# Kernel optimization log

Hardware: AMD Instinct MI355X
Metric: run time of the kernel (lower is better)

## Reference

```python
import jax, jax.numpy as jnp
import numpy as np

B = 65536  # batch size


def setup_inputs() -> dict:
    key = jax.random.key(0)
    ks = jax.random.split(key, 8)
    x = jax.random.normal(ks[0], (B, 784), dtype=jnp.float32)
    conv_w = jax.random.normal(ks[1], (3, 3), dtype=jnp.float32)
    w1 = jax.random.normal(ks[2], (676, 256), dtype=jnp.float32) * 0.04
    b1 = jnp.zeros((256,), dtype=jnp.float32)
    w2 = jax.random.normal(ks[3], (256, 128), dtype=jnp.float32) * 0.06
    b2 = jnp.zeros((128,), dtype=jnp.float32)
    w3 = jax.random.normal(ks[4], (128, 10), dtype=jnp.float32) * 0.09
    b3 = jnp.zeros((10,), dtype=jnp.float32)
    return {"x": x, "conv_w": conv_w, "w1": w1, "b1": b1,
            "w2": w2, "b2": b2, "w3": w3, "b3": b3}


def reference(x, conv_w, w1, b1, w2, b2, w3, b3):
    # x: [B, 784] -> images [B, 1, 28, 28]
    img = x.reshape(-1, 1, 28, 28)
    # Convolve() is a valid cross-correlation (tensordot of window with kernel,
    # no flip) -> lax.conv_general_dilated (also no kernel flip).
    kern = conv_w.reshape(1, 1, 3, 3)  # [O, I, kh, kw]
    y = jax.lax.conv_general_dilated(
        img, kern, window_strides=(1, 1), padding="VALID",
        dimension_numbers=("NCHW", "OIHW", "NCHW"))  # [B, 1, 26, 26]
    h = y.reshape(y.shape[0], 26 * 26)
    h = jax.nn.relu(h @ w1 + b1)
    h = jax.nn.relu(h @ w2 + b2)
    return h @ w3 + b3  # [B, 10] logits
```

## Files before the change

kernel.cpp:

```cpp
#include <hip/hip_runtime.h>
#include <hip/hip_bf16.h>

typedef __bf16 bf16x8 __attribute__((ext_vector_type(8)));
typedef float  f32x4  __attribute__((ext_vector_type(4)));

#define B_ROWS 65536
#define MR 32
#define H0S 712
#define H1S 264
#define H2S 136
#define KC1 22
#define KC2 8
#define KC3 4

#define W1B_ELEMS (704*256)
#define W2B_ELEMS (256*128)
#define W3B_ELEMS (128*16)

__global__ void pack_weights(const float* __restrict__ w1,
                             const float* __restrict__ w2,
                             const float* __restrict__ w3,
                             __hip_bfloat16* __restrict__ w1b,
                             __hip_bfloat16* __restrict__ w2b,
                             __hip_bfloat16* __restrict__ w3b) {
    int idx = blockIdx.x * 256 + threadIdx.x;
    if (idx < W1B_ELEMS) {
        int ki = idx & 31, t = idx >> 5;
        int n = t & 255, kc = t >> 8;
        int k = kc * 32 + ki;
        float v = (k < 676) ? w1[k * 256 + n] : 0.0f;
        w1b[idx] = __float2bfloat16(v);
    } else if (idx < W1B_ELEMS + W2B_ELEMS) {
        int j = idx - W1B_ELEMS;
        int ki = j & 31, t = j >> 5;
        int n = t & 127, kc = t >> 7;
        w2b[j] = __float2bfloat16(w2[(kc * 32 + ki) * 128 + n]);
    } else if (idx < W1B_ELEMS + W2B_ELEMS + W3B_ELEMS) {
        int j = idx - W1B_ELEMS - W2B_ELEMS;
        int ki = j & 31, t = j >> 5;
        int n = t & 15, kc = t >> 4;
        float v = (n < 10) ? w3[(kc * 32 + ki) * 10 + n] : 0.0f;
        w3b[j] = __float2bfloat16(v);
    }
}

__global__ __launch_bounds__(256, 2)
void fused_model(const float* __restrict__ x, const float* __restrict__ cw,
                 const __hip_bfloat16* __restrict__ w1b, const float* __restrict__ b1,
                 const __hip_bfloat16* __restrict__ w2b, const float* __restrict__ b2,
                 const __hip_bfloat16* __restrict__ w3b, const float* __restrict__ b3,
                 float* __restrict__ out) {
    __shared__ __align__(16) char smem[MR * H0S * 2 + MR * H1S * 2];
    __hip_bfloat16* h0s = (__hip_bfloat16*)smem;
    __hip_bfloat16* h1s = (__hip_bfloat16*)(smem + MR * H0S * 2);
    __hip_bfloat16* h2s = (__hip_bfloat16*)smem;

    const int tid = threadIdx.x;
    const int r0  = blockIdx.x * MR;

    const float c00 = cw[0], c01 = cw[1], c02 = cw[2];
    const float c10 = cw[3], c11 = cw[4], c12 = cw[5];
    const float c20 = cw[6], c21 = cw[7], c22 = cw[8];

    for (int t = tid; t < MR * 26; t += 256) {
        int r = t / 26;
        int i = t - r * 26;
        const float* xr = x + (size_t)(r0 + r) * 784 + i * 28;
        float4 v[21];
        #pragma unroll
        for (int di = 0; di < 3; di++) {
            const float4* p4 = (const float4*)(xr + di * 28);
            #pragma unroll
            for (int q = 0; q < 7; q++) v[di * 7 + q] = p4[q];
        }
        #pragma unroll
        for (int k = 0; k < 21; k++)
            asm volatile("" :: "v"(v[k].x), "v"(v[k].y), "v"(v[k].z), "v"(v[k].w));
        float rb[3][28];
        #pragma unroll
        for (int di = 0; di < 3; di++) {
            #pragma unroll
            for (int q = 0; q < 7; q++) {
                rb[di][q*4+0] = v[di*7+q].x; rb[di][q*4+1] = v[di*7+q].y;
                rb[di][q*4+2] = v[di*7+q].z; rb[di][q*4+3] = v[di*7+q].w;
            }
        }
        __hip_bfloat162* hp = (__hip_bfloat162*)(h0s + r * H0S + i * 26);
        #pragma unroll
        for (int k = 0; k < 13; k++) {
            const int j0 = 2 * k, j1 = 2 * k + 1;
            float a0 = c00*rb[0][j0] + c01*rb[0][j0+1] + c02*rb[0][j0+2]
                     + c10*rb[1][j0] + c11*rb[1][j0+1] + c12*rb[1][j0+2]
                     + c20*rb[2][j0] + c21*rb[2][j0+1] + c22*rb[2][j0+2];
            float a1 = c00*rb[0][j1] + c01*rb[0][j1+1] + c02*rb[0][j1+2]
                     + c10*rb[1][j1] + c11*rb[1][j1+1] + c12*rb[1][j1+2]
                     + c20*rb[2][j1] + c21*rb[2][j1+1] + c22*rb[2][j1+2];
            __hip_bfloat162 pr;
            pr.x = __float2bfloat16(a0);
            pr.y = __float2bfloat16(a1);
            hp[k] = pr;
        }
    }
    for (int t = tid; t < MR * 18; t += 256) {
        int r = t / 18;
        int c = t - r * 18;
        ((uint*)(h0s + r * H0S + 676))[c] = 0u;
    }
    __syncthreads();

    const int wave = tid >> 6;
    const int lane = tid & 63;
    const int l15  = lane & 15;
    const int g    = lane >> 4;

    {
        f32x4 acc[2][4];
        #pragma unroll
        for (int mt = 0; mt < 2; mt++)
            #pragma unroll
            for (int nt = 0; nt < 4; nt++)
                acc[mt][nt] = (f32x4){0.f, 0.f, 0.f, 0.f};
        const int nb = wave * 64;
        bf16x8 ab[3][2], bb[3][4];
        #pragma unroll
        for (int p = 0; p < 2; p++) {
            #pragma unroll
            for (int mt = 0; mt < 2; mt++)
                ab[p][mt] = *(const bf16x8*)(h0s + (mt * 16 + l15) * H0S + p * 32 + g * 8);
            #pragma unroll
            for (int nt = 0; nt < 4; nt++)
                bb[p][nt] = *(const bf16x8*)(w1b + ((p * 256 + nb + nt * 16 + l15) * 32 + g * 8));
        }
        #pragma unroll
        for (int kc = 0; kc < KC1; kc++) {
            const int cur = kc % 3;
            const int nxt = (kc + 2) % 3;
            if (kc + 2 < KC1) {
                #pragma unroll
                for (int mt = 0; mt < 2; mt++)
                    ab[nxt][mt] = *(const bf16x8*)(h0s + (mt * 16 + l15) * H0S + (kc + 2) * 32 + g * 8);
                #pragma unroll
                for (int nt = 0; nt < 4; nt++)
                    bb[nxt][nt] = *(const bf16x8*)(w1b + (((kc + 2) * 256 + nb + nt * 16 + l15) * 32 + g * 8));
            }
            #pragma unroll
            for (int mt = 0; mt < 2; mt++)
                #pragma unroll
                for (int nt = 0; nt < 4; nt++)
                    acc[mt][nt] = __builtin_amdgcn_mfma_f32_16x16x32_bf16(
                        ab[cur][mt], bb[cur][nt], acc[mt][nt], 0, 0, 0);
        }
        #pragma unroll
        for (int nt = 0; nt < 4; nt++) {
            const int n = nb + nt * 16 + l15;
            const float bias = b1[n];
            #pragma unroll
            for (int mt = 0; mt < 2; mt++) {
                #pragma unroll
                for (int q = 0; q < 4; q++) {
                    const int row = mt * 16 + g * 4 + q;
                    float v = acc[mt][nt][q] + bias;
                    h1s[row * H1S + n] = __float2bfloat16(fmaxf(v, 0.0f));
                }
            }
        }
    }
    __syncthreads();

    {
        f32x4 acc[2][2];
        #pragma unroll
        for (int mt = 0; mt < 2; mt++)
            #pragma unroll
            for (int nt = 0; nt < 2; nt++)
                acc[mt][nt] = (f32x4){0.f, 0.f, 0.f, 0.f};
        const int nb = wave * 32;
        bf16x8 ab[3][2], bb[3][2];
        #pragma unroll
        for (int p = 0; p < 2; p++) {
            #pragma unroll
            for (int mt = 0; mt < 2; mt++)
                ab[p][mt] = *(const bf16x8*)(h1s + (mt * 16 + l15) * H1S + p * 32 + g * 8);
            #pragma unroll
            for (int nt = 0; nt < 2; nt++)
                bb[p][nt] = *(const bf16x8*)(w2b + ((p * 128 + nb + nt * 16 + l15) * 32 + g * 8));
        }
        #pragma unroll
        for (int kc = 0; kc < KC2; kc++) {
            const int cur = kc % 3;
            const int nxt = (kc + 2) % 3;
            if (kc + 2 < KC2) {
                #pragma unroll
                for (int mt = 0; mt < 2; mt++)
                    ab[nxt][mt] = *(const bf16x8*)(h1s + (mt * 16 + l15) * H1S + (kc + 2) * 32 + g * 8);
                #pragma unroll
                for (int nt = 0; nt < 2; nt++)
                    bb[nxt][nt] = *(const bf16x8*)(w2b + (((kc + 2) * 128 + nb + nt * 16 + l15) * 32 + g * 8));
            }
            #pragma unroll
            for (int mt = 0; mt < 2; mt++)
                #pragma unroll
                for (int nt = 0; nt < 2; nt++)
                    acc[mt][nt] = __builtin_amdgcn_mfma_f32_16x16x32_bf16(
                        ab[cur][mt], bb[cur][nt], acc[mt][nt], 0, 0, 0);
        }
        #pragma unroll
        for (int nt = 0; nt < 2; nt++) {
            const int n = nb + nt * 16 + l15;
            const float bias = b2[n];
            #pragma unroll
            for (int mt = 0; mt < 2; mt++) {
                #pragma unroll
                for (int q = 0; q < 4; q++) {
                    const int row = mt * 16 + g * 4 + q;
                    float v = acc[mt][nt][q] + bias;
                    h2s[row * H2S + n] = __float2bfloat16(fmaxf(v, 0.0f));
                }
            }
        }
    }
    __syncthreads();

    if (wave < 2) {
        f32x4 acc3 = (f32x4){0.f, 0.f, 0.f, 0.f};
        #pragma unroll
        for (int kc = 0; kc < KC3; kc++) {
            bf16x8 a = *(const bf16x8*)(h2s + (wave * 16 + l15) * H2S + kc * 32 + g * 8);
            bf16x8 b = *(const bf16x8*)(w3b + ((kc * 16 + l15) * 32 + g * 8));
            acc3 = __builtin_amdgcn_mfma_f32_16x16x32_bf16(a, b, acc3, 0, 0, 0);
        }
        if (l15 < 10) {
            const float bias = b3[l15];
            #pragma unroll
            for (int q = 0; q < 4; q++) {
                const int row = wave * 16 + g * 4 + q;
                out[(size_t)(r0 + row) * 10 + l15] = acc3[q] + bias;
            }
        }
    }
}

extern "C" void kernel_launch(void* const* d_in, const int* in_sizes, int n_in,
                              void* d_out, int out_size, void* d_ws, size_t ws_size,
                              hipStream_t stream) {
    const float* x  = (const float*)d_in[0];
    const float* cw = (const float*)d_in[1];
    const float* w1 = (const float*)d_in[2];
    const float* b1 = (const float*)d_in[3];
    const float* w2 = (const float*)d_in[4];
    const float* b2 = (const float*)d_in[5];
    const float* w3 = (const float*)d_in[6];
    const float* b3 = (const float*)d_in[7];
    float* out = (float*)d_out;

    __hip_bfloat16* w1b = (__hip_bfloat16*)d_ws;
    __hip_bfloat16* w2b = w1b + W1B_ELEMS;
    __hip_bfloat16* w3b = w2b + W2B_ELEMS;

    const int pack_total = W1B_ELEMS + W2B_ELEMS + W3B_ELEMS;
    pack_weights<<<(pack_total + 255) / 256, 256, 0, stream>>>(w1, w2, w3, w1b, w2b, w3b);
    fused_model<<<B_ROWS / MR, 256, 0, stream>>>(x, cw, w1b, b1, w2b, b2, w3b, b3, out);
}
```

Before: 338.9 us.

## Stage input images in LDS with coalesced loads and register prefetch for conv

The convolution stage used to have each thread read three full input rows straight from global memory, with strided, redundant accesses. Now each wave loads one whole image at a time using coalesced float4 loads into a per-wave LDS staging buffer placed in the still-unused h1 region, prefetching the next image into registers while computing. The 3x3 convolution is then computed from LDS, with two lanes per output row. This cuts redundant and uncoalesced global traffic. In exchange it adds LDS traffic, scalar bf16 stores, an 8-step serial loop per wave, and it relies on in-order LDS access within a wave without an explicit barrier.

New measurement: 333.3 us. Within noise of the previous version (-1.6%).

```diff
diff --git a/kernel.cpp b/kernel.cpp
--- a/kernel.cpp
+++ b/kernel.cpp
@@ -12,6 +12,8 @@
 #define KC1 22
 #define KC2 8
 #define KC3 4
+#define STW 29
+#define STG_FLOATS (28*STW)
 
 #define W1B_ELEMS (704*256)
 #define W2B_ELEMS (256*128)
@@ -55,50 +57,65 @@
     __hip_bfloat16* h1s = (__hip_bfloat16*)(smem + MR * H0S * 2);
     __hip_bfloat16* h2s = (__hip_bfloat16*)smem;
 
-    const int tid = threadIdx.x;
-    const int r0  = blockIdx.x * MR;
+    const int tid  = threadIdx.x;
+    const int r0   = blockIdx.x * MR;
+    const int wave = tid >> 6;
+    const int lane = tid & 63;
 
     const float c00 = cw[0], c01 = cw[1], c02 = cw[2];
     const float c10 = cw[3], c11 = cw[4], c12 = cw[5];
     const float c20 = cw[6], c21 = cw[7], c22 = cw[8];
 
-    for (int t = tid; t < MR * 26; t += 256) {
-        int r = t / 26;
-        int i = t - r * 26;
-        const float* xr = x + (size_t)(r0 + r) * 784 + i * 28;
-        float4 v[21];
-        #pragma unroll
-        for (int di = 0; di < 3; di++) {
-            const float4* p4 = (const float4*)(xr + di * 28);
-            #pragma unroll
-            for (int q = 0; q < 7; q++) v[di * 7 + q] = p4[q];
-        }
-        #pragma unroll
-        for (int k = 0; k < 21; k++)
-            asm volatile("" :: "v"(v[k].x), "v"(v[k].y), "v"(v[k].z), "v"(v[k].w));
-        float rb[3][28];
-        #pragma unroll
-        for (int di = 0; di < 3; di++) {
-            #pragma unroll
-            for (int q = 0; q < 7; q++) {
-                rb[di][q*4+0] = v[di*7+q].x; rb[di][q*4+1] = v[di*7+q].y;
-                rb[di][q*4+2] = v[di*7+q].z; rb[di][q*4+3] = v[di*7+q].w;
-            }
-        }
-        __hip_bfloat162* hp = (__hip_bfloat162*)(h0s + r * H0S + i * 26);
-        #pragma unroll
-        for (int k = 0; k < 13; k++) {
-            const int j0 = 2 * k, j1 = 2 * k + 1;
-            float a0 = c00*rb[0][j0] + c01*rb[0][j0+1] + c02*rb[0][j0+2]
-                     + c10*rb[1][j0] + c11*rb[1][j0+1] + c12*rb[1][j0+2]
-                     + c20*rb[2][j0] + c21*rb[2][j0+1] + c22*rb[2][j0+2];
-            float a1 = c00*rb[0][j1] + c01*rb[0][j1+1] + c02*rb[0][j1+2]
-                     + c10*rb[1][j1] + c11*rb[1][j1+1] + c12*rb[1][j1+2]
-                     + c20*rb[2][j1] + c21*rb[2][j1+1] + c22*rb[2][j1+2];
-            __hip_bfloat162 pr;
-            pr.x = __float2bfloat16(a0);
-            pr.y = __float2bfloat16(a1);
-            hp[k] = pr;
+    {
+        float* stg = ((float*)(smem + MR * H0S * 2)) + wave * STG_FLOATS;
+        float4 rg[4];
+        {
+            const float4* xb = (const float4*)(x + (size_t)(r0 + wave * 8) * 784);
+            #pragma unroll
+            for (int q = 0; q < 4; q++) {
+                int fidx = q * 64 + lane;
+                rg[q] = xb[fidx < 196 ? fidx : 195];
+            }
+        }
+        for (int gi = 0; gi < 8; gi++) {
+            #pragma unroll
+            for (int q = 0; q < 4; q++) {
+                int fidx = q * 64 + lane;
+                if (fidx < 196) {
+                    int row = fidx / 7, c4 = (fidx - row * 7) * 4;
+                    float* p = stg + row * STW + c4;
+                    p[0] = rg[q].x; p[1] = rg[q].y; p[2] = rg[q].z; p[3] = rg[q].w;
+                }
+            }
+            if (gi < 7) {
+                const float4* xb = (const float4*)(x + (size_t)(r0 + wave * 8 + gi + 1) * 784);
+                #pragma unroll
+                for (int q = 0; q < 4; q++) {
+                    int fidx = q * 64 + lane;
+                    rg[q] = xb[fidx < 196 ? fidx : 195];
+                }
+            }
+            if (lane < 52) {
+                const int i  = lane >> 1;
+                const int c0 = (lane & 1) * 13;
+                const float* s0 = stg + i * STW + c0;
+                float w0[15], w1r[15], w2r[15];
+                #pragma unroll
+                for (int c = 0; c < 15; c++) {
+                    w0[c]  = s0[c];
+                    w1r[c] = s0[STW + c];
+                    w2r[c] = s0[2 * STW + c];
+                }
+                const int r = wave * 8 + gi;
+                __hip_bfloat16* hp = h0s + r * H0S + i * 26 + c0;
+                #pragma unroll
+                for (int jj = 0; jj < 13; jj++) {
+                    float a = c00 * w0[jj]  + c01 * w0[jj + 1]  + c02 * w0[jj + 2]
+                            + c10 * w1r[jj] + c11 * w1r[jj + 1] + c12 * w1r[jj + 2]
+                            + c20 * w2r[jj] + c21 * w2r[jj + 1] + c22 * w2r[jj + 2];
+                    hp[jj] = __float2bfloat16(a);
+                }
+            }
         }
     }
     for (int t = tid; t < MR * 18; t += 256) {
@@ -108,10 +125,8 @@
     }
     __syncthreads();
 
-    const int wave = tid >> 6;
-    const int lane = tid & 63;
-    const int l15  = lane & 15;
-    const int g    = lane >> 4;
+    const int l15 = lane & 15;
+    const int g   = lane >> 4;
 
     {
         f32x4 acc[2][4];
```

## Split conv into separate kernel and stage swizzled W1 panels in LDS

Applied to the files above, without the earlier changes.

Splits the fused model into a conv kernel that writes the bf16 conv output (padded to 704) to workspace, and a GEMM kernel with 64-row tiles. The GEMM stages each 32-wide K panel of W1 into LDS in an XOR-swizzled layout shared by all four waves, instead of each wave reading W1 from global memory. The aim is less redundant global W1 traffic and more MFMA work per block. The cost is an extra round trip of roughly 90MB of activations through HBM and two barriers per K step. The old fused path is kept as a fallback when the workspace is too small.

Measured after the change: 446.5 us. 1.32x slower.

```diff
diff --git a/kernel.cpp b/kernel.cpp
--- a/kernel.cpp
+++ b/kernel.cpp
@@ -5,17 +5,22 @@
 typedef float  f32x4  __attribute__((ext_vector_type(4)));
 
 #define B_ROWS 65536
-#define MR 32
-#define H0S 712
-#define H1S 264
-#define H2S 136
 #define KC1 22
 #define KC2 8
 #define KC3 4
-
+#define H1S 264
+#define H2S 136
+#define PANEL_B 16384
 #define W1B_ELEMS (704*256)
 #define W2B_ELEMS (256*128)
 #define W3B_ELEMS (128*16)
+#define W1B_BYTES (KC1*PANEL_B)
+#define WS_WEIGHTS (W1B_BYTES + W2B_ELEMS*2 + W3B_ELEMS*2)
+#define H0B_BYTES ((size_t)B_ROWS*704*2)
+#define GM 64
+
+#define MR 32
+#define H0S 712
 
 __global__ void pack_weights(const float* __restrict__ w1,
                              const float* __restrict__ w2,
@@ -29,7 +34,8 @@
         int n = t & 255, kc = t >> 8;
         int k = kc * 32 + ki;
         float v = (k < 676) ? w1[k * 256 + n] : 0.0f;
-        w1b[idx] = __float2bfloat16(v);
+        size_t byte = (size_t)kc * PANEL_B + (size_t)((n * 64 + ki * 2) ^ ((n & 7) << 4));
+        *(__hip_bfloat16*)((char*)w1b + byte) = __float2bfloat16(v);
     } else if (idx < W1B_ELEMS + W2B_ELEMS) {
         int j = idx - W1B_ELEMS;
         int ki = j & 31, t = j >> 5;
@@ -44,6 +50,228 @@
     }
 }
 
+template<int S>
+__device__ __forceinline__ void conv_body(
+        const float* __restrict__ xr, __hip_bfloat16* __restrict__ hp,
+        float c00, float c01, float c02, float c10, float c11, float c12,
+        float c20, float c21, float c22) {
+    float4 v[3][4];
+    #pragma unroll
+    for (int d = 0; d < 3; d++) {
+        const float4* p4 = (const float4*)(xr + d * 28);
+        #pragma unroll
+        for (int q = 0; q < 4; q++) v[d][q] = p4[S * 3 + q];
+    }
+    #pragma unroll
+    for (int d = 0; d < 3; d++)
+        #pragma unroll
+        for (int q = 0; q < 4; q++)
+            asm volatile("" :: "v"(v[d][q].x), "v"(v[d][q].y), "v"(v[d][q].z), "v"(v[d][q].w));
+    float rb[3][16];
+    #pragma unroll
+    for (int d = 0; d < 3; d++)
+        #pragma unroll
+        for (int q = 0; q < 4; q++) {
+            rb[d][q*4+0] = v[d][q].x; rb[d][q*4+1] = v[d][q].y;
+            rb[d][q*4+2] = v[d][q].z; rb[d][q*4+3] = v[d][q].w;
+        }
+    #pragma unroll
+    for (int jj = 0; jj < 13; jj++) {
+        float a = c00*rb[0][S+jj] + c01*rb[0][S+jj+1] + c02*rb[0][S+jj+2]
+                + c10*rb[1][S+jj] + c11*rb[1][S+jj+1] + c12*rb[1][S+jj+2]
+                + c20*rb[2][S+jj] + c21*rb[2][S+jj+1] + c22*rb[2][S+jj+2];
+        hp[jj] = __float2bfloat16(a);
+    }
+}
+
+__global__ __launch_bounds__(256, 4)
+void conv_kernel(const float* __restrict__ x, const float* __restrict__ cw,
+                 __hip_bfloat16* __restrict__ h0b) {
+    const int tid  = threadIdx.x;
+    const int half = tid >> 7;
+    const int u    = blockIdx.x * 128 + (tid & 127);
+    const int i    = u % 26;
+    const int r    = u / 26;
+    const float c00 = cw[0], c01 = cw[1], c02 = cw[2];
+    const float c10 = cw[3], c11 = cw[4], c12 = cw[5];
+    const float c20 = cw[6], c21 = cw[7], c22 = cw[8];
+    const float* xr = x + (size_t)r * 784 + i * 28;
+    __hip_bfloat16* hp = h0b + (size_t)r * 704 + i * 26 + half * 13;
+    if (half == 0) conv_body<0>(xr, hp, c00, c01, c02, c10, c11, c12, c20, c21, c22);
+    else           conv_body<1>(xr, hp, c00, c01, c02, c10, c11, c12, c20, c21, c22);
+    if (half == 1 && i == 25) {
+        uint* pz = (uint*)(h0b + (size_t)r * 704 + 676);
+        #pragma unroll
+        for (int q = 0; q < 14; q++) pz[q] = 0u;
+    }
+}
+
+__global__ __launch_bounds__(256, 2)
+void gemm_kernel(const __hip_bfloat16* __restrict__ h0b,
+                 const __hip_bfloat16* __restrict__ w1b, const float* __restrict__ b1,
+                 const __hip_bfloat16* __restrict__ w2b, const float* __restrict__ b2,
+                 const __hip_bfloat16* __restrict__ w3b, const float* __restrict__ b3,
+                 float* __restrict__ out) {
+    __shared__ __align__(16) char smem[17408 + GM * H1S * 2];
+    char* bpan = smem;
+    __hip_bfloat16* h2s = (__hip_bfloat16*)smem;
+    __hip_bfloat16* h1s = (__hip_bfloat16*)(smem + 17408);
+
+    const int tid  = threadIdx.x;
+    const int r0   = blockIdx.x * GM;
+    const int wave = tid >> 6;
+    const int lane = tid & 63;
+    const int l15  = lane & 15;
+    const int g    = lane >> 4;
+    const char* w1c = (const char*)w1b;
+
+    {
+        const int mh = wave >> 1, nh = wave & 1;
+        const __hip_bfloat16* arow0 = h0b + (size_t)(r0 + mh * 32 + l15) * 704;
+        const __hip_bfloat16* arow1 = arow0 + (size_t)16 * 704;
+
+        float4 st[4];
+        #pragma unroll
+        for (int j = 0; j < 4; j++)
+            st[j] = *(const float4*)(w1c + 0 * PANEL_B + j * 4096 + tid * 16);
+        #pragma unroll
+        for (int j = 0; j < 4; j++)
+            *(float4*)(bpan + j * 4096 + tid * 16) = st[j];
+
+        bf16x8 ar[4][2];
+        #pragma unroll
+        for (int p = 0; p < 3; p++) {
+            ar[p][0] = *(const bf16x8*)(arow0 + p * 32 + g * 8);
+            ar[p][1] = *(const bf16x8*)(arow1 + p * 32 + g * 8);
+        }
+        f32x4 acc[2][8];
+        #pragma unroll
+        for (int mt = 0; mt < 2; mt++)
+            #pragma unroll
+            for (int nt = 0; nt < 8; nt++)
+                acc[mt][nt] = (f32x4){0.f, 0.f, 0.f, 0.f};
+        __syncthreads();
+
+        #pragma unroll
+        for (int kc = 0; kc < KC1; kc++) {
+            if (kc + 1 < KC1) {
+                #pragma unroll
+                for (int j = 0; j < 4; j++)
+                    st[j] = *(const float4*)(w1c + (size_t)(kc + 1) * PANEL_B + j * 4096 + tid * 16);
+            }
+            if (kc + 3 < KC1) {
+                const int sl = (kc + 3) & 3;
+                ar[sl][0] = *(const bf16x8*)(arow0 + (kc + 3) * 32 + g * 8);
+                ar[sl][1] = *(const bf16x8*)(arow1 + (kc + 3) * 32 + g * 8);
+            }
+            bf16x8 bb[8];
+            #pragma unroll
+            for (int nt = 0; nt < 8; nt++) {
+                const int n = nh * 128 + nt * 16 + l15;
+                const int off = (n * 64 + g * 16) ^ ((n & 7) << 4);
+                bb[nt] = *(const bf16x8*)(bpan + off);
+            }
+            const int cs = kc & 3;
+            #pragma unroll
+            for (int mt = 0; mt < 2; mt++)
+                #pragma unroll
+                for (int nt = 0; nt < 8; nt++)
+                    acc[mt][nt] = __builtin_amdgcn_mfma_f32_16x16x32_bf16(
+                        ar[cs][mt], bb[nt], acc[mt][nt], 0, 0, 0);
+            __syncthreads();
+            if (kc + 1 < KC1) {
+                #pragma unroll
+                for (int j = 0; j < 4; j++)
+                    *(float4*)(bpan + j * 4096 + tid * 16) = st[j];
+                __syncthreads();
+            }
+        }
+        #pragma unroll
+        for (int nt = 0; nt < 8; nt++) {
+            const int n = nh * 128 + nt * 16 + l15;
+            const float bias = b1[n];
+            #pragma unroll
+            for (int mt = 0; mt < 2; mt++) {
+                #pragma unroll
+                for (int q = 0; q < 4; q++) {
+                    const int row = mh * 32 + mt * 16 + g * 4 + q;
+                    float v = acc[mt][nt][q] + bias;
+                    h1s[row * H1S + n] = __float2bfloat16(fmaxf(v, 0.0f));
+                }
+            }
+        }
+    }
+    __syncthreads();
+
+    {
+        f32x4 acc[4][2];
+        #pragma unroll
+        for (int mt = 0; mt < 4; mt++)
+            #pragma unroll
+            for (int nt = 0; nt < 2; nt++)
+                acc[mt][nt] = (f32x4){0.f, 0.f, 0.f, 0.f};
+        const int nb = wave * 32;
+        bf16x8 bb2[3][2];
+        #pragma unroll
+        for (int p = 0; p < 2; p++)
+            #pragma unroll
+            for (int nt = 0; nt < 2; nt++)
+                bb2[p][nt] = *(const bf16x8*)(w2b + ((p * 128 + nb + nt * 16 + l15) * 32 + g * 8));
+        #pragma unroll
+        for (int kc = 0; kc < KC2; kc++) {
+            const int cur = kc % 3, nxt = (kc + 2) % 3;
+            if (kc + 2 < KC2) {
+                #pragma unroll
+                for (int nt = 0; nt < 2; nt++)
+                    bb2[nxt][nt] = *(const bf16x8*)(w2b + (((kc + 2) * 128 + nb + nt * 16 + l15) * 32 + g * 8));
+            }
+            bf16x8 ab[4];
+            #pragma unroll
+            for (int mt = 0; mt < 4; mt++)
+                ab[mt] = *(const bf16x8*)(h1s + (mt * 16 + l15) * H1S + kc * 32 + g * 8);
+            #pragma unroll
+            for (int mt = 0; mt < 4; mt++)
+                #pragma unroll
+                for (int nt = 0; nt < 2; nt++)
+                    acc[mt][nt] = __builtin_amdgcn_mfma_f32_16x16x32_bf16(
+                        ab[mt], bb2[cur][nt], acc[mt][nt], 0, 0, 0);
+        }
+        #pragma unroll
+        for (int nt = 0; nt < 2; nt++) {
+            const int n = nb + nt * 16 + l15;
+            const float bias = b2[n];
+            #pragma unroll
+            for (int mt = 0; mt < 4; mt++) {
+                #pragma unroll
+                for (int q = 0; q < 4; q++) {
+                    const int row = mt * 16 + g * 4 + q;
+                    float v = acc[mt][nt][q] + bias;
+                    h2s[row * H2S + n] = __float2bfloat16(fmaxf(v, 0.0f));
+                }
+            }
+        }
+    }
+    __syncthreads();
+
+    {
+        f32x4 acc3 = (f32x4){0.f, 0.f, 0.f, 0.f};
+        #pragma unroll
+        for (int kc = 0; kc < KC3; kc++) {
+            bf16x8 a = *(const bf16x8*)(h2s + (wave * 16 + l15) * H2S + kc * 32 + g * 8);
+            bf16x8 b = *(const bf16x8*)(w3b + ((kc * 16 + l15) * 32 + g * 8));
+            acc3 = __builtin_amdgcn_mfma_f32_16x16x32_bf16(a, b, acc3, 0, 0, 0);
+        }
+        if (l15 < 10) {
+            const float bias = b3[l15];
+            #pragma unroll
+            for (int q = 0; q < 4; q++) {
+                const int row = wave * 16 + g * 4 + q;
+                out[(size_t)(r0 + row) * 10 + l15] = acc3[q] + bias;
+            }
+        }
+    }
+}
+
 __global__ __launch_bounds__(256, 2)
 void fused_model(const float* __restrict__ x, const float* __restrict__ cw,
                  const __hip_bfloat16* __restrict__ w1b, const float* __restrict__ b1,
@@ -54,6 +282,7 @@
     __hip_bfloat16* h0s = (__hip_bfloat16*)smem;
     __hip_bfloat16* h1s = (__hip_bfloat16*)(smem + MR * H0S * 2);
     __hip_bfloat16* h2s = (__hip_bfloat16*)smem;
+    const char* w1c = (const char*)w1b;
 
     const int tid = threadIdx.x;
     const int r0  = blockIdx.x * MR;
@@ -128,8 +357,11 @@
             for (int mt = 0; mt < 2; mt++)
                 ab[p][mt] = *(const bf16x8*)(h0s + (mt * 16 + l15) * H0S + p * 32 + g * 8);
             #pragma unroll
-            for (int nt = 0; nt < 4; nt++)
-                bb[p][nt] = *(const bf16x8*)(w1b + ((p * 256 + nb + nt * 16 + l15) * 32 + g * 8));
+            for (int nt = 0; nt < 4; nt++) {
+                const int n = nb + nt * 16 + l15;
+                bb[p][nt] = *(const bf16x8*)(w1c + (size_t)p * PANEL_B
+                                + ((n * 64 + g * 16) ^ ((n & 7) << 4)));
+            }
         }
         #pragma unroll
         for (int kc = 0; kc < KC1; kc++) {
@@ -140,8 +372,11 @@
                 for (int mt = 0; mt < 2; mt++)
                     ab[nxt][mt] = *(const bf16x8*)(h0s + (mt * 16 + l15) * H0S + (kc + 2) * 32 + g * 8);
                 #pragma unroll
-                for (int nt = 0; nt < 4; nt++)
-                    bb[nxt][nt] = *(const bf16x8*)(w1b + (((kc + 2) * 256 + nb + nt * 16 + l15) * 32 + g * 8));
+                for (int nt = 0; nt < 4; nt++) {
+                    const int n = nb + nt * 16 + l15;
+                    bb[nxt][nt] = *(const bf16x8*)(w1c + (size_t)(kc + 2) * PANEL_B
+                                    + ((n * 64 + g * 16) ^ ((n & 7) << 4)));
+                }
             }
             #pragma unroll
             for (int mt = 0; mt < 2; mt++)
@@ -254,10 +489,18 @@
     float* out = (float*)d_out;
 
     __hip_bfloat16* w1b = (__hip_bfloat16*)d_ws;
-    __hip_bfloat16* w2b = w1b + W1B_ELEMS;
+    __hip_bfloat16* w2b = (__hip_bfloat16*)((char*)d_ws + W1B_BYTES);
     __hip_bfloat16* w3b = w2b + W2B_ELEMS;
 
     const int pack_total = W1B_ELEMS + W2B_ELEMS + W3B_ELEMS;
     pack_weights<<<(pack_total + 255) / 256, 256, 0, stream>>>(w1, w2, w3, w1b, w2b, w3b);
-    fused_model<<<B_ROWS / MR, 256, 0, stream>>>(x, cw, w1b, b1, w2b, b2, w3b, b3, out);
+
+    const size_t need = (size_t)WS_WEIGHTS + H0B_BYTES;
+    if (ws_size >= need) {
+        __hip_bfloat16* h0b = (__hip_bfloat16*)((char*)d_ws + WS_WEIGHTS);
+        conv_kernel<<<B_ROWS * 26 / 128, 256, 0, stream>>>(x, cw, h0b);
+        gemm_kernel<<<B_ROWS / GM, 256, 0, stream>>>(h0b, w1b, b1, w2b, b2, w3b, b3, out);
+    } else {
+        fused_model<<<B_ROWS / MR, 256, 0, stream>>>(x, cw, w1b, b1, w2b, b2, w3b, b3, out);
+    }
 }
```
